# Kernel optimization log

Measured on AMD Instinct MI355X. Metric: run time of the kernel, lower is better.

The kernel has to match this reference:

```python
import jax, jax.numpy as jnp
import numpy as np

B, S, H, L, NH, FF, V, NL = 16, 512, 768, 12, 12, 3072, 30522, 9
DH = H // NH


def setup_inputs() -> dict:
    key = jax.random.key(0)
    ks = iter(jax.random.split(key, 16))
    def w(shape, scale=0.02):
        return jax.random.normal(next(ks), shape, jnp.float32) * scale
    return {
        "input_word_ids": jax.random.randint(next(ks), (B, S), 0, V, jnp.int32),
        "input_mask": jnp.ones((B, S), jnp.int32),
        "input_type_ids": jnp.zeros((B, S), jnp.int32),
        "valid_mask": jax.random.randint(next(ks), (B, S), 0, 2, jnp.int32),
        "word_emb": w((V, H)),
        "pos_emb": w((S, H)),
        "type_emb": w((2, H)),
        "emb_ln_g": jnp.ones((H,), jnp.float32),
        "emb_ln_b": jnp.zeros((H,), jnp.float32),
        "Wq": w((L, H, H)), "bq": jnp.zeros((L, H), jnp.float32),
        "Wk": w((L, H, H)), "bk": jnp.zeros((L, H), jnp.float32),
        "Wv": w((L, H, H)), "bv": jnp.zeros((L, H), jnp.float32),
        "Wo": w((L, H, H)), "bo": jnp.zeros((L, H), jnp.float32),
        "ln1_g": jnp.ones((L, H), jnp.float32), "ln1_b": jnp.zeros((L, H), jnp.float32),
        "W1": w((L, H, FF)), "b1": jnp.zeros((L, FF), jnp.float32),
        "W2": w((L, FF, H)), "b2": jnp.zeros((L, H), jnp.float32),
        "ln2_g": jnp.ones((L, H), jnp.float32), "ln2_b": jnp.zeros((L, H), jnp.float32),
        "cls_W": w((H, NL)), "cls_b": jnp.zeros((NL,), jnp.float32),
    }


def _layer_norm(x, g, b):
    m = x.mean(-1, keepdims=True)
    v = ((x - m) ** 2).mean(-1, keepdims=True)
    return (x - m) * jax.lax.rsqrt(v + 1e-12) * g + b


def reference(input_word_ids, input_mask, input_type_ids, valid_mask,
              word_emb, pos_emb, type_emb, emb_ln_g, emb_ln_b,
              Wq, bq, Wk, bk, Wv, bv, Wo, bo, ln1_g, ln1_b,
              W1, b1, W2, b2, ln2_g, ln2_b, cls_W, cls_b):
    b, s = input_word_ids.shape
    # --- BERT embeddings ---
    x = word_emb[input_word_ids] + pos_emb[None, :s] + type_emb[input_type_ids]
    x = _layer_norm(x, emb_ln_g, emb_ln_b)  # [B,S,H]
    attn_bias = (1.0 - input_mask.astype(jnp.float32))[:, None, None, :] * -1e9
    scale = 1.0 / np.sqrt(DH).astype(np.float32)

    def step(h, p):
        wq, bq_, wk, bk_, wv, bv_, wo, bo_, g1, gb1, w1, wb1, w2, wb2, g2, gb2 = p
        q = (h @ wq + bq_).reshape(b, s, NH, DH)
        k = (h @ wk + bk_).reshape(b, s, NH, DH)
        v = (h @ wv + bv_).reshape(b, s, NH, DH)
        scores = jnp.einsum('bqhd,bkhd->bhqk', q, k) * scale + attn_bias
        probs = jax.nn.softmax(scores, axis=-1)
        ctx = jnp.einsum('bhqk,bkhd->bqhd', probs, v).reshape(b, s, H)
        h = _layer_norm(h + ctx @ wo + bo_, g1, gb1)
        ff = jax.nn.gelu(h @ w1 + wb1, approximate=False)
        h = _layer_norm(h + ff @ w2 + wb2, g2, gb2)
        return h, None

    params = (Wq, bq, Wk, bk, Wv, bv, Wo, bo, ln1_g, ln1_b, W1, b1, W2, b2, ln2_g, ln2_b)
    x, _ = jax.lax.scan(step, x, params)

    # --- valid-token compaction (vectorized form of the python double loop) ---
    # valid tokens packed to the front (stable order), remainder zero-padded
    invalid = (1 - valid_mask).astype(jnp.int32)
    perm = jnp.argsort(invalid, axis=1, stable=True)          # [B,S]
    compact = jnp.take_along_axis(x, perm[:, :, None], axis=1)
    counts = valid_mask.sum(axis=1)                           # [B]
    keep = (jnp.arange(s)[None, :] < counts[:, None])[:, :, None]
    compact = jnp.where(keep, compact, jnp.zeros((), x.dtype))
    # dropout is identity at inference (training=False)
    logits = jax.nn.softmax(compact @ cls_W + cls_b, axis=-1)  # [B,S,NL]
    return logits
```

## Files before the change

### kernel.cpp

```cpp
#include <hip/hip_runtime.h>
#include <cstdint>
#include <cstddef>

#define B_ 16
#define S_ 512
#define H_ 768
#define L_ 12
#define NH_ 12
#define DH_ 64
#define FF_ 3072
#define NL_ 9
#define QKV_ 2304

typedef _Float16 f16x8 __attribute__((ext_vector_type(8)));
typedef _Float16 f16x4 __attribute__((ext_vector_type(4)));
typedef float f32x4 __attribute__((ext_vector_type(4)));

__device__ __forceinline__ void load_lds16(const void* g, void* l) {
  __builtin_amdgcn_global_load_lds(
      (const __attribute__((address_space(1))) unsigned int*)g,
      (__attribute__((address_space(3))) unsigned int*)l, 16, 0, 0);
}

__device__ __forceinline__ float block_sum256(float v, float* red) {
#pragma unroll
  for (int off = 32; off; off >>= 1) v += __shfl_down(v, off);
  __syncthreads();
  if ((threadIdx.x & 63) == 0) red[threadIdx.x >> 6] = v;
  __syncthreads();
  return red[0] + red[1] + red[2] + red[3];
}

__device__ __forceinline__ float block_sum192(float v, float* red) {
#pragma unroll
  for (int off = 32; off; off >>= 1) v += __shfl_down(v, off);
  __syncthreads();
  if ((threadIdx.x & 63) == 0) red[threadIdx.x >> 6] = v;
  __syncthreads();
  return red[0] + red[1] + red[2];
}

__device__ __forceinline__ float gelu_f(float x) {
  float au = fabsf(x) * 0.70710678118654752f;
  float t = 1.0f / (1.0f + 0.3275911f * au);
  float p = ((((1.061405429f * t - 1.453152027f) * t + 1.421413741f) * t
              - 0.284496736f) * t + 0.254829592f) * t;
  float e = p * __expf(-au * au);
  float phi = (x >= 0.0f) ? (1.0f - 0.5f * e) : (0.5f * e);
  return x * phi;
}

__global__ __launch_bounds__(256) void embed_ln_kernel(
    const int* __restrict__ wid, const int* __restrict__ tpid,
    const float* __restrict__ we, const float* __restrict__ pe,
    const float* __restrict__ te, const float* __restrict__ g,
    const float* __restrict__ bb, _Float16* __restrict__ hb) {
  __shared__ float red[4];
  int tok = blockIdx.x;
  int s = tok & (S_ - 1);
  int w = wid[tok], tp = tpid[tok];
  int t = threadIdx.x;
  float x[3];
#pragma unroll
  for (int i = 0; i < 3; ++i) {
    int j = t + i * 256;
    x[i] = we[(size_t)w * H_ + j] + pe[(size_t)s * H_ + j] + te[(size_t)tp * H_ + j];
  }
  float m = block_sum256(x[0] + x[1] + x[2], red) * (1.0f / H_);
  float d0 = x[0] - m, d1 = x[1] - m, d2 = x[2] - m;
  float var = block_sum256(d0 * d0 + d1 * d1 + d2 * d2, red) * (1.0f / H_);
  float rs = rsqrtf(var + 1e-12f);
#pragma unroll
  for (int i = 0; i < 3; ++i) {
    int j = t + i * 256;
    float v = (x[i] - m) * rs * g[j] + bb[j];
    hb[(size_t)tok * H_ + j] = (_Float16)v;
  }
}

__global__ __launch_bounds__(192) void ln_f16_kernel(
    const _Float16* __restrict__ x, const float* __restrict__ g,
    const float* __restrict__ bb, _Float16* __restrict__ hb) {
  __shared__ float red[3];
  int tok = blockIdx.x;
  int t = threadIdx.x;
  int j = t * 4;
  f16x4 xv = *(const f16x4*)&x[(size_t)tok * H_ + j];
  float v0 = (float)xv[0], v1 = (float)xv[1], v2 = (float)xv[2], v3 = (float)xv[3];
  float m = block_sum192(v0 + v1 + v2 + v3, red) * (1.0f / H_);
  float d0 = v0 - m, d1 = v1 - m, d2 = v2 - m, d3 = v3 - m;
  __syncthreads();
  float var = block_sum192(d0 * d0 + d1 * d1 + d2 * d2 + d3 * d3, red) * (1.0f / H_);
  float rs = rsqrtf(var + 1e-12f);
  float4 gv = *(const float4*)&g[j];
  float4 bv = *(const float4*)&bb[j];
  f16x4 o;
  o[0] = (_Float16)(d0 * rs * gv.x + bv.x);
  o[1] = (_Float16)(d1 * rs * gv.y + bv.y);
  o[2] = (_Float16)(d2 * rs * gv.z + bv.z);
  o[3] = (_Float16)(d3 * rs * gv.w + bv.w);
  *(f16x4*)&hb[(size_t)tok * H_ + j] = o;
}

__global__ __launch_bounds__(256) void convert_weights_kernel(
    const float* __restrict__ Wq, const float* __restrict__ Wk,
    const float* __restrict__ Wv, const float* __restrict__ Wo,
    const float* __restrict__ W1, const float* __restrict__ W2,
    _Float16* __restrict__ qT, _Float16* __restrict__ kT,
    _Float16* __restrict__ vT, _Float16* __restrict__ oT,
    _Float16* __restrict__ w1T, _Float16* __restrict__ w2T,
    const float* __restrict__ bq, const float* __restrict__ bk,
    const float* __restrict__ bv, float* __restrict__ qkvb) {
  int id = blockIdx.x;
  int tid = threadIdx.x;
  if (id == 1728) {
    for (int j = tid; j < H_; j += 256) {
      qkvb[j] = bq[j];
      qkvb[H_ + j] = bk[j];
      qkvb[2 * H_ + j] = bv[j];
    }
    return;
  }
  __shared__ float T[64][65];
  const float* src;
  _Float16* dst;
  int K, N, tk, tn;
  if (id < 576) {
    int mat = id / 144, t = id % 144;
    K = 768; N = 768; tk = t / 12; tn = t % 12;
    src = (mat == 0) ? Wq : (mat == 1) ? Wk : (mat == 2) ? Wv : Wo;
    dst = (mat == 0) ? qT : (mat == 1) ? kT : (mat == 2) ? vT : oT;
  } else if (id < 1152) {
    int t = id - 576; K = 768; N = 3072; tk = t / 48; tn = t % 48;
    src = W1; dst = w1T;
  } else {
    int t = id - 1152; K = 3072; N = 768; tk = t / 12; tn = t % 12;
    src = W2; dst = w2T;
  }
  int k0 = tk * 64, n0 = tn * 64;
  {
    int r = tid >> 4, c4 = (tid & 15) * 4;
#pragma unroll
    for (int i = 0; i < 4; ++i) {
      float4 v = *(const float4*)&src[(size_t)(k0 + r + i * 16) * N + n0 + c4];
      T[r + i * 16][c4 + 0] = v.x;
      T[r + i * 16][c4 + 1] = v.y;
      T[r + i * 16][c4 + 2] = v.z;
      T[r + i * 16][c4 + 3] = v.w;
    }
  }
  __syncthreads();
#pragma unroll
  for (int i = 0; i < 2; ++i) {
    int chunk = tid + i * 256;
    int n = chunk >> 3, kc = (chunk & 7) * 8;
    f16x8 o;
#pragma unroll
    for (int j = 0; j < 8; ++j) o[j] = (_Float16)T[kc + j][n];
    *(f16x8*)&dst[(size_t)(n0 + n) * K + k0 + kc] = o;
  }
}

template <int OUT>
__global__ __launch_bounds__(256) void gemm_f16(
    const _Float16* __restrict__ A, const _Float16* __restrict__ Bt,
    const float* __restrict__ bias, void* __restrict__ Cv,
    int M, int N, int K, const _Float16* __restrict__ hres) {
  __shared__ _Float16 As[2][128 * 64];
  __shared__ _Float16 Bs[2][128 * 64];
  int tid = threadIdx.x;
  int lane = tid & 63, w = tid >> 6;
  int wr = w >> 1, wc = w & 1;
  int l15 = lane & 15, kb = lane >> 4;
  int swr = l15 & 7;

  int nwg = gridDim.x * gridDim.y;
  int bid = blockIdx.y * gridDim.x + blockIdx.x;
  int swz = bid;
  if ((nwg & 7) == 0) {
    int cpx = nwg >> 3;
    swz = (bid & 7) * cpx + (bid >> 3);
  }
  int bx = swz % gridDim.x, by = swz / gridDim.x;
  int row0 = by * 128, col0 = bx * 128;

  int drow = lane >> 3;
  int schunk = (lane & 7) ^ drow;
  const _Float16* gA = A + (size_t)(row0 + w * 32 + drow) * K + schunk * 8;
  const _Float16* gB = Bt + (size_t)(col0 + w * 32 + drow) * K + schunk * 8;

  auto STAGE = [&](int t, int buf) {
    int ko = t * 64;
#pragma unroll
    for (int j = 0; j < 4; ++j) {
      load_lds16(gA + (size_t)(j * 8) * K + ko,
                 (char*)&As[buf][0] + (w * 32 + j * 8) * 128);
      load_lds16(gB + (size_t)(j * 8) * K + ko,
                 (char*)&Bs[buf][0] + (w * 32 + j * 8) * 128);
    }
  };

  f32x4 acc[4][4] = {};
  int nk = K >> 6;

  STAGE(0, 0);
  __syncthreads();

  for (int kt = 0; kt < nk; ++kt) {
    int cur = kt & 1;
    if (kt + 1 < nk) STAGE(kt + 1, cur ^ 1);
#pragma unroll
    for (int ks = 0; ks < 2; ++ks) {
      f16x8 af[4], bf[4];
      int rpos = ((ks * 4 + kb) ^ swr) * 8;
#pragma unroll
      for (int m = 0; m < 4; ++m)
        af[m] = *(const f16x8*)&As[cur][(wr * 64 + m * 16 + l15) * 64 + rpos];
#pragma unroll
      for (int n = 0; n < 4; ++n)
        bf[n] = *(const f16x8*)&Bs[cur][(wc * 64 + n * 16 + l15) * 64 + rpos];
#pragma unroll
      for (int m = 0; m < 4; ++m)
#pragma unroll
        for (int n = 0; n < 4; ++n)
          acc[m][n] = __builtin_amdgcn_mfma_f32_16x16x32_f16(af[m], bf[n], acc[m][n], 0, 0, 0);
    }
    __syncthreads();
  }
#pragma unroll
  for (int n = 0; n < 4; ++n) {
    int col = col0 + wc * 64 + n * 16 + l15;
    float bv = bias[col];
#pragma unroll
    for (int m = 0; m < 4; ++m) {
      int rowb = row0 + wr * 64 + m * 16 + kb * 4;
#pragma unroll
      for (int r = 0; r < 4; ++r) {
        float v = acc[m][n][r] + bv;
        if (OUT == 2) v = gelu_f(v);
        if (OUT == 3) v += (float)hres[(size_t)(rowb + r) * N + col];
        ((_Float16*)Cv)[(size_t)(rowb + r) * N + col] = (_Float16)v;
      }
    }
  }
}

template <int OUT>
__global__ __launch_bounds__(128) void gemm64(
    const _Float16* __restrict__ A, const _Float16* __restrict__ Bt,
    const float* __restrict__ bias, void* __restrict__ Cv,
    int M, int N, int K, const _Float16* __restrict__ hres) {
  __shared__ _Float16 As[2][64 * 64];
  __shared__ _Float16 Bs[2][128 * 64];
  int tid = threadIdx.x;
  int lane = tid & 63, w = tid >> 6;
  int l15 = lane & 15, kb = lane >> 4;
  int swr = l15 & 7;

  int nwg = gridDim.x * gridDim.y;
  int bid = blockIdx.y * gridDim.x + blockIdx.x;
  int swz = bid;
  if ((nwg & 7) == 0) {
    int cpx = nwg >> 3;
    swz = (bid & 7) * cpx + (bid >> 3);
  }
  int bx = swz % gridDim.x, by = swz / gridDim.x;
  int row0 = by * 64, col0 = bx * 128;

  int drow = lane >> 3;
  int schunk = (lane & 7) ^ drow;
  const _Float16* gA = A + (size_t)(row0 + w * 32 + drow) * K + schunk * 8;
  const _Float16* gB = Bt + (size_t)(col0 + w * 64 + drow) * K + schunk * 8;

  auto STAGE = [&](int t, int buf) {
    int ko = t * 64;
#pragma unroll
    for (int j = 0; j < 4; ++j)
      load_lds16(gA + (size_t)(j * 8) * K + ko,
                 (char*)&As[buf][0] + (w * 32 + j * 8) * 128);
#pragma unroll
    for (int j = 0; j < 8; ++j)
      load_lds16(gB + (size_t)(j * 8) * K + ko,
                 (char*)&Bs[buf][0] + (w * 64 + j * 8) * 128);
  };

  f32x4 acc[4][4] = {};
  int nk = K >> 6;

  STAGE(0, 0);
  __syncthreads();

  for (int kt = 0; kt < nk; ++kt) {
    int cur = kt & 1;
    if (kt + 1 < nk) STAGE(kt + 1, cur ^ 1);
#pragma unroll
    for (int ks = 0; ks < 2; ++ks) {
      f16x8 af[4], bf[4];
      int rpos = ((ks * 4 + kb) ^ swr) * 8;
#pragma unroll
      for (int m = 0; m < 4; ++m)
        af[m] = *(const f16x8*)&As[cur][(m * 16 + l15) * 64 + rpos];
#pragma unroll
      for (int n = 0; n < 4; ++n)
        bf[n] = *(const f16x8*)&Bs[cur][(w * 64 + n * 16 + l15) * 64 + rpos];
#pragma unroll
      for (int m = 0; m < 4; ++m)
#pragma unroll
        for (int n = 0; n < 4; ++n)
          acc[m][n] = __builtin_amdgcn_mfma_f32_16x16x32_f16(af[m], bf[n], acc[m][n], 0, 0, 0);
    }
    __syncthreads();
  }
#pragma unroll
  for (int n = 0; n < 4; ++n) {
    int col = col0 + w * 64 + n * 16 + l15;
    float bv = bias[col];
#pragma unroll
    for (int m = 0; m < 4; ++m) {
      int rowb = row0 + m * 16 + kb * 4;
#pragma unroll
      for (int r = 0; r < 4; ++r) {
        float v = acc[m][n][r] + bv;
        if (OUT == 2) v = gelu_f(v);
        if (OUT == 3) v += (float)hres[(size_t)(rowb + r) * N + col];
        ((_Float16*)Cv)[(size_t)(rowb + r) * N + col] = (_Float16)v;
      }
    }
  }
}

__global__ __launch_bounds__(256) void vtrans_kernel(
    const _Float16* __restrict__ v, int RS, _Float16* __restrict__ vt) {
  __shared__ _Float16 T[64][72];
  int s0 = blockIdx.x * 64;
  int bh = blockIdx.y;
  int b = bh / NH_, h = bh % NH_;
  int tid = threadIdx.x;
#pragma unroll
  for (int i = 0; i < 2; ++i) {
    int chunk = tid + i * 256;
    int s = chunk >> 3, dc = (chunk & 7) * 8;
    *(f16x8*)&T[s][dc] = *(const f16x8*)&v[(size_t)(b * S_ + s0 + s) * RS + h * DH_ + dc];
  }
  __syncthreads();
#pragma unroll
  for (int i = 0; i < 2; ++i) {
    int chunk = tid + i * 256;
    int d = chunk >> 3, sc = (chunk & 7) * 8;
    f16x8 o;
#pragma unroll
    for (int j = 0; j < 8; ++j) o[j] = T[sc + j][d];
    *(f16x8*)&vt[(size_t)(bh * DH_ + d) * S_ + s0 + sc] = o;
  }
}

__global__ __launch_bounds__(256) void flash_attn_kernel(
    const _Float16* __restrict__ q, const _Float16* __restrict__ k,
    const _Float16* __restrict__ vt, int RS, const int* __restrict__ mask,
    _Float16* __restrict__ ctx) {
  __shared__ _Float16 Ks[128 * 72];
  __shared__ _Float16 Vs[64 * 136];
  __shared__ _Float16 Ps[4][16 * 136];
  __shared__ float biasz[S_];
  int qt = blockIdx.x, h = blockIdx.y, b = blockIdx.z;
  int tid = threadIdx.x, lane = tid & 63, w = tid >> 6;
  int l15 = lane & 15, kb = lane >> 4;
  const float C = 0.125f * 1.44269504088896f;

  for (int i = tid; i < S_; i += 256)
    biasz[i] = (1.0f - (float)mask[b * S_ + i]) * (-1e9f * C);

  int qrow = b * S_ + qt * 64 + w * 16 + l15;
  f16x8 qf[2];
  qf[0] = *(const f16x8*)&q[(size_t)qrow * RS + h * DH_ + kb * 8];
  qf[1] = *(const f16x8*)&q[(size_t)qrow * RS + h * DH_ + 32 + kb * 8];

  auto loadKV = [&](int kt, f16x8* rk, f16x8* rv) {
#pragma unroll
    for (int i = 0; i < 4; ++i) {
      int idx = tid + i * 256;
      int r = idx >> 3, c = idx & 7;
      rk[i] = *(const f16x8*)&k[(size_t)(b * S_ + kt * 128 + r) * RS + h * DH_ + c * 8];
      int d = idx >> 4, c2 = idx & 15;
      rv[i] = *(const f16x8*)&vt[(size_t)((b * NH_ + h) * DH_ + d) * S_ + kt * 128 + c2 * 8];
    }
  };

  float m_run[4], l_run[4];
  f32x4 o[4] = {};
#pragma unroll
  for (int r = 0; r < 4; ++r) { m_run[r] = -1e30f; l_run[r] = 0.f; }

  f16x8 rk[4], rv[4];
  loadKV(0, rk, rv);
  for (int kt = 0; kt < 4; ++kt) {
    __syncthreads();
#pragma unroll
    for (int i = 0; i < 4; ++i) {
      int idx = tid + i * 256;
      int r = idx >> 3, c = idx & 7;
      *(f16x8*)&Ks[r * 72 + c * 8] = rk[i];
      int d = idx >> 4, c2 = idx & 15;
      *(f16x8*)&Vs[d * 136 + c2 * 8] = rv[i];
    }
    __syncthreads();
    if (kt < 3) loadKV(kt + 1, rk, rv);
    f32x4 s[8];
#pragma unroll
    for (int nf = 0; nf < 8; ++nf) {
      f16x8 b0 = *(const f16x8*)&Ks[(nf * 16 + l15) * 72 + kb * 8];
      f16x8 b1 = *(const f16x8*)&Ks[(nf * 16 + l15) * 72 + 32 + kb * 8];
      f32x4 z = {};
      z = __builtin_amdgcn_mfma_f32_16x16x32_f16(qf[0], b0, z, 0, 0, 0);
      z = __builtin_amdgcn_mfma_f32_16x16x32_f16(qf[1], b1, z, 0, 0, 0);
      s[nf] = z;
    }
    float zb[8];
#pragma unroll
    for (int nf = 0; nf < 8; ++nf) zb[nf] = biasz[kt * 128 + nf * 16 + l15];
    float pw[8][4];
    float corr[4];
#pragma unroll
    for (int r = 0; r < 4; ++r) {
      float mx = -1e30f;
#pragma unroll
      for (int nf = 0; nf < 8; ++nf) mx = fmaxf(mx, s[nf][r] * C + zb[nf]);
#pragma unroll
      for (int d = 1; d < 16; d <<= 1) mx = fmaxf(mx, __shfl_xor(mx, d));
      float mnew = fmaxf(m_run[r], mx);
      float cr = exp2f(m_run[r] - mnew);
      m_run[r] = mnew;
      corr[r] = cr;
      float sum = 0.f;
#pragma unroll
      for (int nf = 0; nf < 8; ++nf) {
        float pv = exp2f(s[nf][r] * C + zb[nf] - mnew);
        pw[nf][r] = pv;
        sum += pv;
      }
#pragma unroll
      for (int d = 1; d < 16; d <<= 1) sum += __shfl_xor(sum, d);
      l_run[r] = l_run[r] * cr + sum;
    }
#pragma unroll
    for (int nf2 = 0; nf2 < 4; ++nf2)
#pragma unroll
      for (int r = 0; r < 4; ++r) o[nf2][r] *= corr[r];
#pragma unroll
    for (int nf = 0; nf < 8; ++nf)
#pragma unroll
      for (int r = 0; r < 4; ++r)
        Ps[w][(kb * 4 + r) * 136 + nf * 16 + l15] = (_Float16)pw[nf][r];
#pragma unroll
    for (int ks = 0; ks < 4; ++ks) {
      f16x8 pa = *(const f16x8*)&Ps[w][l15 * 136 + ks * 32 + kb * 8];
#pragma unroll
      for (int nf2 = 0; nf2 < 4; ++nf2) {
        f16x8 vb2 = *(const f16x8*)&Vs[(nf2 * 16 + l15) * 136 + ks * 32 + kb * 8];
        o[nf2] = __builtin_amdgcn_mfma_f32_16x16x32_f16(pa, vb2, o[nf2], 0, 0, 0);
      }
    }
  }
  float inv[4];
#pragma unroll
  for (int r = 0; r < 4; ++r) inv[r] = 1.0f / fmaxf(l_run[r], 1e-37f);
#pragma unroll
  for (int nf2 = 0; nf2 < 4; ++nf2)
#pragma unroll
    for (int r = 0; r < 4; ++r) {
      int row = b * S_ + qt * 64 + w * 16 + kb * 4 + r;
      ctx[(size_t)row * H_ + h * DH_ + nf2 * 16 + l15] = (_Float16)(o[nf2][r] * inv[r]);
    }
}

__global__ void compact_idx_kernel(const int* __restrict__ valid, int* __restrict__ dest) {
  int b = threadIdx.x;
  if (b >= B_) return;
  int cnt = 0;
  for (int s = 0; s < S_; ++s) {
    int vv = valid[b * S_ + s];
    dest[b * S_ + s] = vv ? cnt : -1;
    cnt += vv;
  }
}

__global__ __launch_bounds__(192) void scatter_kernel(
    const _Float16* __restrict__ hb, const int* __restrict__ dest,
    float* __restrict__ compact) {
  int tok = blockIdx.x;
  int d = dest[tok];
  if (d < 0) return;
  int b = tok >> 9;
  int j = threadIdx.x * 4;
  f16x4 v = *(const f16x4*)&hb[(size_t)tok * H_ + j];
  float4 o = {(float)v[0], (float)v[1], (float)v[2], (float)v[3]};
  *(float4*)&compact[((size_t)(b * S_ + d)) * H_ + j] = o;
}

__global__ __launch_bounds__(256) void cls_kernel(
    const float* __restrict__ x, const float* __restrict__ W,
    const float* __restrict__ bias2, float* __restrict__ out) {
  int lane = threadIdx.x & 63, wv = threadIdx.x >> 6;
  int tok = blockIdx.x * 4 + wv;
  float acc[NL_] = {};
  for (int hh = lane; hh < H_; hh += 64) {
    float xv = x[(size_t)tok * H_ + hh];
#pragma unroll
    for (int n = 0; n < NL_; ++n) acc[n] = fmaf(xv, W[hh * NL_ + n], acc[n]);
  }
#pragma unroll
  for (int n = 0; n < NL_; ++n) {
#pragma unroll
    for (int off = 32; off; off >>= 1) acc[n] += __shfl_down(acc[n], off);
  }
  if (lane == 0) {
    float vls[NL_], mx = -1e30f;
#pragma unroll
    for (int n = 0; n < NL_; ++n) {
      vls[n] = acc[n] + bias2[n];
      mx = fmaxf(mx, vls[n]);
    }
    float s = 0.f;
#pragma unroll
    for (int n = 0; n < NL_; ++n) {
      vls[n] = expf(vls[n] - mx);
      s += vls[n];
    }
    float inv = 1.0f / s;
#pragma unroll
    for (int n = 0; n < NL_; ++n) out[(size_t)tok * NL_ + n] = vls[n] * inv;
  }
}

extern "C" void kernel_launch(void* const* d_in, const int* in_sizes, int n_in,
                              void* d_out, int out_size, void* d_ws, size_t ws_size,
                              hipStream_t stream) {
  const int* wid = (const int*)d_in[0];
  const int* mask = (const int*)d_in[1];
  const int* tpid = (const int*)d_in[2];
  const int* valid = (const int*)d_in[3];
  const float* we = (const float*)d_in[4];
  const float* pe = (const float*)d_in[5];
  const float* te = (const float*)d_in[6];
  const float* eg = (const float*)d_in[7];
  const float* eb = (const float*)d_in[8];
  const float* Wq = (const float*)d_in[9];
  const float* bq = (const float*)d_in[10];
  const float* Wk = (const float*)d_in[11];
  const float* bk = (const float*)d_in[12];
  const float* Wv = (const float*)d_in[13];
  const float* bv = (const float*)d_in[14];
  const float* Wo = (const float*)d_in[15];
  const float* bo = (const float*)d_in[16];
  const float* g1 = (const float*)d_in[17];
  const float* gb1 = (const float*)d_in[18];
  const float* W1 = (const float*)d_in[19];
  const float* bf1 = (const float*)d_in[20];
  const float* W2 = (const float*)d_in[21];
  const float* bf2 = (const float*)d_in[22];
  const float* g2 = (const float*)d_in[23];
  const float* gb2 = (const float*)d_in[24];
  const float* cW = (const float*)d_in[25];
  const float* cb = (const float*)d_in[26];
  float* out = (float*)d_out;

  const size_t TOK = (size_t)B_ * S_;
  char* ws = (char*)d_ws;
  _Float16* hb = (_Float16*)(ws + 25165824);
  _Float16* t1h = (_Float16*)(ws + 37748736);
  char* un1 = ws + 62914560;
  _Float16* qkv = (_Float16*)un1;
  _Float16* vt = (_Float16*)(un1 + 37748736);
  _Float16* ffh = (_Float16*)un1;
  float* compactf = (float*)un1;
  _Float16* ctx = (_Float16*)(ws + 113246208);
  char* wbuf = ws + 125829120;
  _Float16* wqT = (_Float16*)wbuf;
  _Float16* wkT = (_Float16*)(wbuf + 1179648);
  _Float16* wvT = (_Float16*)(wbuf + 2359296);
  _Float16* woT = (_Float16*)(wbuf + 3538944);
  _Float16* w1T = (_Float16*)(wbuf + 4718592);
  _Float16* w2T = (_Float16*)(wbuf + 9437184);
  int* dest = (int*)(ws + 139984896);
  float* qkvb = (float*)(ws + 140017664);

  dim3 blk(256);
  dim3 blk192(192);
  dim3 blk128(128);
  embed_ln_kernel<<<dim3((unsigned)TOK), blk, 0, stream>>>(wid, tpid, we, pe, te, eg, eb, hb);

  dim3 gQKV64(QKV_ / 128, TOK / 64);
  dim3 gH64(H_ / 128, TOK / 64);
  dim3 gF(FF_ / 128, TOK / 128);
  for (int l = 0; l < L_; ++l) {
    convert_weights_kernel<<<dim3(1729), blk, 0, stream>>>(
        Wq + (size_t)l * H_ * H_, Wk + (size_t)l * H_ * H_,
        Wv + (size_t)l * H_ * H_, Wo + (size_t)l * H_ * H_,
        W1 + (size_t)l * H_ * FF_, W2 + (size_t)l * FF_ * H_,
        wqT, wkT, wvT, woT, w1T, w2T,
        bq + l * H_, bk + l * H_, bv + l * H_, qkvb);
    gemm64<1><<<gQKV64, blk128, 0, stream>>>(hb, wqT, qkvb, qkv, (int)TOK, QKV_, H_, nullptr);
    vtrans_kernel<<<dim3(S_ / 64, B_ * NH_), blk, 0, stream>>>(qkv + 2 * H_, QKV_, vt);
    flash_attn_kernel<<<dim3(S_ / 64, NH_, B_), blk, 0, stream>>>(
        qkv, qkv + H_, vt, QKV_, mask, ctx);
    gemm64<3><<<gH64, blk128, 0, stream>>>(ctx, woT, bo + l * H_, t1h, (int)TOK, H_, H_, hb);
    ln_f16_kernel<<<dim3((unsigned)TOK), blk192, 0, stream>>>(t1h, g1 + l * H_, gb1 + l * H_, hb);
    gemm_f16<2><<<gF, blk, 0, stream>>>(hb, w1T, bf1 + l * FF_, ffh, (int)TOK, FF_, H_, nullptr);
    gemm64<3><<<gH64, blk128, 0, stream>>>(ffh, w2T, bf2 + l * H_, t1h, (int)TOK, H_, FF_, hb);
    ln_f16_kernel<<<dim3((unsigned)TOK), blk192, 0, stream>>>(t1h, g2 + l * H_, gb2 + l * H_, hb);
  }

  compact_idx_kernel<<<1, 64, 0, stream>>>(valid, dest);
  hipMemsetAsync(compactf, 0, TOK * H_ * sizeof(float), stream);
  scatter_kernel<<<dim3((unsigned)TOK), blk192, 0, stream>>>(hb, dest, compactf);
  cls_kernel<<<dim3((unsigned)(TOK / 4)), blk, 0, stream>>>(compactf, cW, cb, out);
}
```

Measured before the change: 3.370 ms.

## Fuse compaction gather into classifier and parallelize compaction index computation

Replaces the serial per-batch compaction loop with a ballot/popcount prefix scan over 512 threads per batch. The classifier now reads the fp16 hidden states directly through a source-index map, so the fp32 memset and scatter passes are gone. The attention mask bias is computed once by a new kernel instead of being recomputed in every attention block of every layer. This removes roughly 50MB of memset and scatter traffic plus a single-thread serial scan. It adds one small kernel launch.

```diff
diff --git a/kernel.cpp b/kernel.cpp
--- a/kernel.cpp
+++ b/kernel.cpp
@@ -14,6 +14,7 @@
 
 typedef _Float16 f16x8 __attribute__((ext_vector_type(8)));
 typedef _Float16 f16x4 __attribute__((ext_vector_type(4)));
+typedef _Float16 f16x2 __attribute__((ext_vector_type(2)));
 typedef float f32x4 __attribute__((ext_vector_type(4)));
 
 __device__ __forceinline__ void load_lds16(const void* g, void* l) {
@@ -161,6 +162,12 @@
   }
 }
 
+__global__ void maskbias_kernel(const int* __restrict__ mask, float* __restrict__ bz) {
+  int i = blockIdx.x * 256 + threadIdx.x;
+  const float C = 0.125f * 1.44269504088896f;
+  bz[i] = (1.0f - (float)mask[i]) * (-1e9f * C);
+}
+
 template <int OUT>
 __global__ __launch_bounds__(256) void gemm_f16(
     const _Float16* __restrict__ A, const _Float16* __restrict__ Bt,
@@ -356,7 +363,7 @@
 
 __global__ __launch_bounds__(256) void flash_attn_kernel(
     const _Float16* __restrict__ q, const _Float16* __restrict__ k,
-    const _Float16* __restrict__ vt, int RS, const int* __restrict__ mask,
+    const _Float16* __restrict__ vt, int RS, const float* __restrict__ biasz_g,
     _Float16* __restrict__ ctx) {
   __shared__ _Float16 Ks[128 * 72];
   __shared__ _Float16 Vs[64 * 136];
@@ -367,8 +374,7 @@
   int l15 = lane & 15, kb = lane >> 4;
   const float C = 0.125f * 1.44269504088896f;
 
-  for (int i = tid; i < S_; i += 256)
-    biasz[i] = (1.0f - (float)mask[b * S_ + i]) * (-1e9f * C);
+  for (int i = tid; i < S_; i += 256) biasz[i] = biasz_g[b * S_ + i];
 
   int qrow = b * S_ + qt * 64 + w * 16 + l15;
   f16x8 qf[2];
@@ -473,40 +479,40 @@
     }
 }
 
-__global__ void compact_idx_kernel(const int* __restrict__ valid, int* __restrict__ dest) {
-  int b = threadIdx.x;
-  if (b >= B_) return;
-  int cnt = 0;
-  for (int s = 0; s < S_; ++s) {
-    int vv = valid[b * S_ + s];
-    dest[b * S_ + s] = vv ? cnt : -1;
-    cnt += vv;
-  }
-}
-
-__global__ __launch_bounds__(192) void scatter_kernel(
-    const _Float16* __restrict__ hb, const int* __restrict__ dest,
-    float* __restrict__ compact) {
-  int tok = blockIdx.x;
-  int d = dest[tok];
-  if (d < 0) return;
-  int b = tok >> 9;
-  int j = threadIdx.x * 4;
-  f16x4 v = *(const f16x4*)&hb[(size_t)tok * H_ + j];
-  float4 o = {(float)v[0], (float)v[1], (float)v[2], (float)v[3]};
-  *(float4*)&compact[((size_t)(b * S_ + d)) * H_ + j] = o;
+__global__ __launch_bounds__(512) void compact_idx_kernel(
+    const int* __restrict__ valid, int* __restrict__ src_of) {
+  __shared__ int wsum[8];
+  int b = blockIdx.x;
+  int t = threadIdx.x;
+  int lane = t & 63, wv = t >> 6;
+  int v = valid[b * S_ + t];
+  unsigned long long ball = __ballot(v != 0);
+  int pre = __popcll(ball & ((1ULL << lane) - 1ULL));
+  if (lane == 0) wsum[wv] = __popcll(ball);
+  src_of[b * S_ + t] = -1;
+  __syncthreads();
+  int base = 0;
+#pragma unroll
+  for (int i = 0; i < 8; ++i) base += (i < wv) ? wsum[i] : 0;
+  if (v) src_of[b * S_ + base + pre] = b * S_ + t;
 }
 
 __global__ __launch_bounds__(256) void cls_kernel(
-    const float* __restrict__ x, const float* __restrict__ W,
-    const float* __restrict__ bias2, float* __restrict__ out) {
+    const _Float16* __restrict__ hb, const int* __restrict__ src_of,
+    const float* __restrict__ W, const float* __restrict__ bias2,
+    float* __restrict__ out) {
   int lane = threadIdx.x & 63, wv = threadIdx.x >> 6;
   int tok = blockIdx.x * 4 + wv;
+  int src = src_of[tok];
   float acc[NL_] = {};
-  for (int hh = lane; hh < H_; hh += 64) {
-    float xv = x[(size_t)tok * H_ + hh];
-#pragma unroll
-    for (int n = 0; n < NL_; ++n) acc[n] = fmaf(xv, W[hh * NL_ + n], acc[n]);
+  if (src >= 0) {
+    for (int h0 = lane * 2; h0 < H_; h0 += 128) {
+      f16x2 xv = *(const f16x2*)&hb[(size_t)src * H_ + h0];
+      float x0 = (float)xv[0], x1 = (float)xv[1];
+#pragma unroll
+      for (int n = 0; n < NL_; ++n)
+        acc[n] = fmaf(x0, W[h0 * NL_ + n], fmaf(x1, W[(h0 + 1) * NL_ + n], acc[n]));
+    }
   }
 #pragma unroll
   for (int n = 0; n < NL_; ++n) {
@@ -572,7 +578,6 @@
   _Float16* qkv = (_Float16*)un1;
   _Float16* vt = (_Float16*)(un1 + 37748736);
   _Float16* ffh = (_Float16*)un1;
-  float* compactf = (float*)un1;
   _Float16* ctx = (_Float16*)(ws + 113246208);
   char* wbuf = ws + 125829120;
   _Float16* wqT = (_Float16*)wbuf;
@@ -581,13 +586,15 @@
   _Float16* woT = (_Float16*)(wbuf + 3538944);
   _Float16* w1T = (_Float16*)(wbuf + 4718592);
   _Float16* w2T = (_Float16*)(wbuf + 9437184);
-  int* dest = (int*)(ws + 139984896);
+  int* src_of = (int*)(ws + 139984896);
   float* qkvb = (float*)(ws + 140017664);
+  float* biasz_g = (float*)(ws + 140026880);
 
   dim3 blk(256);
   dim3 blk192(192);
   dim3 blk128(128);
   embed_ln_kernel<<<dim3((unsigned)TOK), blk, 0, stream>>>(wid, tpid, we, pe, te, eg, eb, hb);
+  maskbias_kernel<<<dim3((unsigned)(TOK / 256)), blk, 0, stream>>>(mask, biasz_g);
 
   dim3 gQKV64(QKV_ / 128, TOK / 64);
   dim3 gH64(H_ / 128, TOK / 64);
@@ -602,7 +609,7 @@
     gemm64<1><<<gQKV64, blk128, 0, stream>>>(hb, wqT, qkvb, qkv, (int)TOK, QKV_, H_, nullptr);
     vtrans_kernel<<<dim3(S_ / 64, B_ * NH_), blk, 0, stream>>>(qkv + 2 * H_, QKV_, vt);
     flash_attn_kernel<<<dim3(S_ / 64, NH_, B_), blk, 0, stream>>>(
-        qkv, qkv + H_, vt, QKV_, mask, ctx);
+        qkv, qkv + H_, vt, QKV_, biasz_g, ctx);
     gemm64<3><<<gH64, blk128, 0, stream>>>(ctx, woT, bo + l * H_, t1h, (int)TOK, H_, H_, hb);
     ln_f16_kernel<<<dim3((unsigned)TOK), blk192, 0, stream>>>(t1h, g1 + l * H_, gb1 + l * H_, hb);
     gemm_f16<2><<<gF, blk, 0, stream>>>(hb, w1T, bf1 + l * FF_, ffh, (int)TOK, FF_, H_, nullptr);
@@ -610,8 +617,6 @@
     ln_f16_kernel<<<dim3((unsigned)TOK), blk192, 0, stream>>>(t1h, g2 + l * H_, gb2 + l * H_, hb);
   }
 
-  compact_idx_kernel<<<1, 64, 0, stream>>>(valid, dest);
-  hipMemsetAsync(compactf, 0, TOK * H_ * sizeof(float), stream);
-  scatter_kernel<<<dim3((unsigned)TOK), blk192, 0, stream>>>(hb, dest, compactf);
-  cls_kernel<<<dim3((unsigned)(TOK / 4)), blk, 0, stream>>>(compactf, cW, cb, out);
-}
+  compact_idx_kernel<<<dim3(B_), dim3(512), 0, stream>>>(valid, src_of);
+  cls_kernel<<<dim3((unsigned)(TOK / 4)), blk, 0, stream>>>(hb, src_of, cW, cb, out);
+}
```

New measurement: 3.353 ms. Within noise of the previous version (-0.5%).
